# Kernel tuning notes

Hardware: AMD Instinct MI355X
Metric: run time of the kernel (lower is better)

## Reference

```python
import jax, jax.numpy as jnp
import numpy as np

N = 50000      # nodes
E = 500000     # edges
IN = 128       # input feature dim
HID = 64       # hidden per-head dim
CLS = 64       # num classes
SLOPE = 0.2    # leaky_relu negative slope


def _gat_layer(x, W, al, ar, src, dst):
    """One GATConv: project, per-edge score, edge-softmax over dst, weighted aggregate.
    x: [N, Din], W: [Din, H*F], al/ar: [H, F]. Returns [N, H, F]."""
    H, F = al.shape
    n = x.shape[0]
    feat = (x @ W).reshape(n, H, F)                      # [N,H,F]
    el = jnp.einsum('nhf,hf->nh', feat, al)              # [N,H]
    er = jnp.einsum('nhf,hf->nh', feat, ar)              # [N,H]
    e = el[src] + er[dst]                                # u_add_v -> [E,H]
    e = jnp.where(e >= 0, e, SLOPE * e)                  # leaky_relu
    # edge_softmax over destination nodes (numerically stable)
    m = jax.lax.stop_gradient(jax.ops.segment_max(e, dst, num_segments=n))
    ex = jnp.exp(e - m[dst])
    denom = jax.ops.segment_sum(ex, dst, num_segments=n)
    a = ex / denom[dst]                                  # [E,H]
    # u_mul_e + sum aggregation
    out = jax.ops.segment_sum(feat[src] * a[:, :, None], dst, num_segments=n)
    return out                                           # [N,H,F]


def setup_inputs() -> dict:
    key = jax.random.key(0)
    ks = jax.random.split(key, 12)
    s = 0.05  # xavier-ish scale
    x = jax.random.normal(ks[0], (N, IN), jnp.float32)
    src = jax.random.randint(ks[1], (E,), 0, N)
    dst = jax.random.randint(ks[2], (E,), 0, N)
    W1 = jax.random.normal(ks[3], (IN, 4 * HID), jnp.float32) * s
    al1 = jax.random.normal(ks[4], (4, HID), jnp.float32) * s
    ar1 = jax.random.normal(ks[5], (4, HID), jnp.float32) * s
    W2 = jax.random.normal(ks[6], (4 * HID, 4 * HID), jnp.float32) * s
    al2 = jax.random.normal(ks[7], (4, HID), jnp.float32) * s
    ar2 = jax.random.normal(ks[8], (4, HID), jnp.float32) * s
    W3 = jax.random.normal(ks[9], (4 * HID, CLS), jnp.float32) * s
    al3 = jax.random.normal(ks[10], (1, CLS), jnp.float32) * s
    ar3 = jax.random.normal(ks[11], (1, CLS), jnp.float32) * s
    res_W3 = jax.random.normal(jax.random.fold_in(key, 99), (4 * HID, CLS), jnp.float32) * s
    return {"x": x, "W1": W1, "al1": al1, "ar1": ar1, "W2": W2, "al2": al2,
            "ar2": ar2, "W3": W3, "al3": al3, "ar3": ar3, "res_W3": res_W3,
            "src": src, "dst": dst}


def reference(x, W1, al1, ar1, W2, al2, ar2, W3, al3, ar3, res_W3, src, dst):
    # layer 0: no residual, elu activation, flatten heads
    h = _gat_layer(x, W1, al1, ar1, src, dst)            # [N,4,64]
    h = jax.nn.elu(h).reshape(N, -1)                     # [N,256]
    # layer 1: residual is Identity (in_dst 256 == 4*64), elu, flatten
    h1 = _gat_layer(h, W2, al2, ar2, src, dst)           # [N,4,64]
    h1 = h1 + h.reshape(N, 4, HID)                       # residual (Identity)
    h = jax.nn.elu(h1).reshape(N, -1)                    # [N,256]
    # layer 2: residual Linear 256->64, no activation, mean over heads
    h2 = _gat_layer(h, W3, al3, ar3, src, dst)           # [N,1,64]
    h2 = h2 + (h @ res_W3).reshape(N, 1, CLS)            # residual fc
    logits = h2.mean(axis=1)                             # [N,64]
    return logits
```

## Files before the change

### kernel.cpp

```cpp
#include <hip/hip_runtime.h>
#include <hip/hip_bf16.h>
#include <math.h>

#define SLOPE 0.2f

typedef __attribute__((ext_vector_type(8))) short short8;
typedef __attribute__((ext_vector_type(4))) float f32x4;

static __device__ __forceinline__ float leakyf(float x) { return x >= 0.f ? x : SLOPE * x; }
static __device__ __forceinline__ float bflo(unsigned u) { return __builtin_bit_cast(float, u << 16); }
static __device__ __forceinline__ float bfhi(unsigned u) { return __builtin_bit_cast(float, u & 0xffff0000u); }

struct __align__(8) bf16x4 { __hip_bfloat16 x, y, z, w; };

__global__ void cvt_bf16(const float* __restrict__ in, __hip_bfloat16* __restrict__ o, int n) {
    int i = (blockIdx.x * blockDim.x + threadIdx.x) * 4;
    if (i + 3 < n) {
        float4 v = *(const float4*)(in + i);
        o[i + 0] = __float2bfloat16(v.x);
        o[i + 1] = __float2bfloat16(v.y);
        o[i + 2] = __float2bfloat16(v.z);
        o[i + 3] = __float2bfloat16(v.w);
    } else {
        for (int j = i; j < n; ++j) o[j] = __float2bfloat16(in[j]);
    }
}

__global__ void tconv(const float* __restrict__ W, __hip_bfloat16* __restrict__ Wt, int K, int Nc) {
    int i = blockIdx.x * blockDim.x + threadIdx.x;
    if (i < K * Nc) {
        int k = i / Nc, n = i - k * Nc;
        Wt[(size_t)n * K + k] = __float2bfloat16(W[i]);
    }
}

template<int HEADS, bool ACC, bool OUT_BF16, bool DO_ATTN>
__global__ __launch_bounds__(256) void gemm_bf16(const __hip_bfloat16* __restrict__ A,
                                                 const __hip_bfloat16* __restrict__ Wt,
                                                 void* __restrict__ outv,
                                                 const float* __restrict__ al,
                                                 const float* __restrict__ ar,
                                                 float* __restrict__ el,
                                                 float* __restrict__ er,
                                                 int M, int K) {
    const int Nc = HEADS * 64;
    const int lane = threadIdx.x & 63;
    const int wid = threadIdx.x >> 6;
    const int rlo = lane & 15;
    const int q = lane >> 4;
    const int kg = q * 8;
    const int head = (HEADS == 4) ? wid : 0;
    const int m0 = (HEADS == 4) ? blockIdx.x * 64 : blockIdx.x * 256 + wid * 64;
    const int cbase = head * 64;

    f32x4 acc[4][4];
#pragma unroll
    for (int mf = 0; mf < 4; ++mf)
#pragma unroll
        for (int nf = 0; nf < 4; ++nf) acc[mf][nf] = (f32x4){0.f, 0.f, 0.f, 0.f};

    for (int k0 = 0; k0 < K; k0 += 32) {
        short8 a[4];
#pragma unroll
        for (int mf = 0; mf < 4; ++mf) {
            int r = m0 + mf * 16 + rlo;
            if (r >= M) r = M - 1;
            a[mf] = *(const short8*)(A + (size_t)r * K + k0 + kg);
        }
#pragma unroll
        for (int nf = 0; nf < 4; ++nf) {
            short8 b = *(const short8*)(Wt + (size_t)(cbase + nf * 16 + rlo) * K + k0 + kg);
#pragma unroll
            for (int mf = 0; mf < 4; ++mf)
                acc[mf][nf] = __builtin_amdgcn_mfma_f32_16x16x32_bf16(a[mf], b, acc[mf][nf], 0, 0, 0);
        }
    }

    float alv[4], arv[4];
    if (DO_ATTN) {
#pragma unroll
        for (int nf = 0; nf < 4; ++nf) {
            alv[nf] = al[cbase + nf * 16 + rlo];
            arv[nf] = ar[cbase + nf * 16 + rlo];
        }
    }

#pragma unroll
    for (int mf = 0; mf < 4; ++mf) {
#pragma unroll
        for (int reg = 0; reg < 4; ++reg) {
            int r = m0 + mf * 16 + q * 4 + reg;
            if (DO_ATTN) {
                float pl = 0.f, pr = 0.f;
#pragma unroll
                for (int nf = 0; nf < 4; ++nf) {
                    pl += acc[mf][nf][reg] * alv[nf];
                    pr += acc[mf][nf][reg] * arv[nf];
                }
#pragma unroll
                for (int off = 1; off < 16; off <<= 1) {
                    pl += __shfl_xor(pl, off);
                    pr += __shfl_xor(pr, off);
                }
                if (rlo == 0 && r < M) {
                    el[(size_t)r * HEADS + head] = pl;
                    er[(size_t)r * HEADS + head] = pr;
                }
            }
            if (r < M) {
#pragma unroll
                for (int nf = 0; nf < 4; ++nf) {
                    int c = cbase + nf * 16 + rlo;
                    float v = acc[mf][nf][reg];
                    if (OUT_BF16) {
                        ((__hip_bfloat16*)outv)[(size_t)r * Nc + c] = __float2bfloat16(v);
                    } else {
                        float* o = (float*)outv + (size_t)r * Nc + c;
                        *o = ACC ? (*o + v) : v;
                    }
                }
            }
        }
    }
}

__global__ void hist_kernel(const int* __restrict__ dst, int* __restrict__ counts, int e) {
    int i = blockIdx.x * blockDim.x + threadIdx.x;
    if (i < e) atomicAdd(&counts[dst[i]], 1);
}

__global__ __launch_bounds__(1024) void scan_block(const int* __restrict__ counts,
                                                   int* __restrict__ offsets,
                                                   int* __restrict__ bsums, int n) {
    __shared__ int ws[16];
    int tid = threadIdx.x, lane = tid & 63, wid = tid >> 6;
    int idx = blockIdx.x * 1024 + tid;
    int v = (idx < n) ? counts[idx] : 0;
    int s = v;
#pragma unroll
    for (int off = 1; off < 64; off <<= 1) {
        int t = __shfl_up(s, off);
        if (lane >= off) s += t;
    }
    if (lane == 63) ws[wid] = s;
    __syncthreads();
    if (tid < 16) {
        int w2 = ws[tid];
#pragma unroll
        for (int off = 1; off < 16; off <<= 1) {
            int t = __shfl_up(w2, off);
            if (tid >= off) w2 += t;
        }
        ws[tid] = w2;
    }
    __syncthreads();
    int wpre = wid ? ws[wid - 1] : 0;
    if (idx < n) offsets[idx] = wpre + s - v;
    if (tid == 0) bsums[blockIdx.x] = ws[15];
}

__global__ void scan_sums(int* bsums, int nb) {
    int lane = threadIdx.x;
    int v = (lane < nb) ? bsums[lane] : 0;
    int s = v;
#pragma unroll
    for (int off = 1; off < 64; off <<= 1) {
        int t = __shfl_up(s, off);
        if (lane >= off) s += t;
    }
    if (lane < nb) bsums[lane] = s - v;
}

__global__ __launch_bounds__(1024) void add_off(const int* __restrict__ bsums,
                                                int* __restrict__ offsets, int n, int e) {
    int idx = blockIdx.x * 1024 + threadIdx.x;
    if (idx < n) offsets[idx] += bsums[blockIdx.x];
    if (idx == 0) offsets[n] = e;
}

__global__ void copy_int_kernel(const int* __restrict__ a, int* __restrict__ b, int n) {
    int i = blockIdx.x * blockDim.x + threadIdx.x;
    if (i < n) b[i] = a[i];
}

__global__ void scatter_kernel(const int* __restrict__ src, const int* __restrict__ dst,
                               int* __restrict__ cursor, int* __restrict__ csr_src, int e) {
    int i = blockIdx.x * blockDim.x + threadIdx.x;
    if (i < e) {
        int pos = atomicAdd(&cursor[dst[i]], 1);
        csr_src[pos] = src[i];
    }
}

template<int H, bool RES, int ACT, bool OUT_BF16>
__global__ __launch_bounds__(256) void gat_agg(const __hip_bfloat16* __restrict__ feat,
                                               const float* __restrict__ el,
                                               const float* __restrict__ er,
                                               const int* __restrict__ offsets,
                                               const int* __restrict__ csr_src,
                                               const __hip_bfloat16* __restrict__ resid,
                                               void* __restrict__ outv, int n) {
    const int D = H * 64;
    int node = blockIdx.x * 4 + (threadIdx.x >> 6);
    int lane = threadIdx.x & 63;
    if (node >= n) return;
    int e0 = offsets[node], e1 = offsets[node + 1];
    const int head = (H == 4) ? (lane >> 4) : 0;
    float erh = er[(size_t)node * H + head];

    float m = -INFINITY, den = 0.f;
    float acc[4] = {0.f, 0.f, 0.f, 0.f};
    const unsigned short* fp = (const unsigned short*)feat;

#define STEP(LV, UX, UY)                                                \
    {                                                                   \
        float xx = leakyf((LV) + erh);                                  \
        float mn = fmaxf(m, xx);                                        \
        float rs = __expf(m - mn);                                      \
        float w = __expf(xx - mn);                                      \
        m = mn;                                                         \
        den = den * rs + w;                                             \
        acc[0] = acc[0] * rs + w * bflo(UX);                            \
        if (H == 4) {                                                   \
            acc[1] = acc[1] * rs + w * bfhi(UX);                        \
            acc[2] = acc[2] * rs + w * bflo(UY);                        \
            acc[3] = acc[3] * rs + w * bfhi(UY);                        \
        }                                                               \
    }

    int e = e0;
    for (; e + 2 <= e1; e += 2) {
        int s0 = csr_src[e], s1 = csr_src[e + 1];
        float l0 = el[(size_t)s0 * H + head];
        float l1 = el[(size_t)s1 * H + head];
        unsigned ux0, uy0 = 0, ux1, uy1 = 0;
        if (H == 4) {
            uint2 u0 = *(const uint2*)(fp + (size_t)s0 * D + lane * 4);
            uint2 u1 = *(const uint2*)(fp + (size_t)s1 * D + lane * 4);
            ux0 = u0.x; uy0 = u0.y; ux1 = u1.x; uy1 = u1.y;
        } else {
            ux0 = fp[(size_t)s0 * D + lane];
            ux1 = fp[(size_t)s1 * D + lane];
        }
        STEP(l0, ux0, uy0);
        STEP(l1, ux1, uy1);
    }
    if (e < e1) {
        int s0 = csr_src[e];
        float l0 = el[(size_t)s0 * H + head];
        unsigned ux0, uy0 = 0;
        if (H == 4) {
            uint2 u0 = *(const uint2*)(fp + (size_t)s0 * D + lane * 4);
            ux0 = u0.x; uy0 = u0.y;
        } else {
            ux0 = fp[(size_t)s0 * D + lane];
        }
        STEP(l0, ux0, uy0);
    }
#undef STEP

    float inv = den > 0.f ? 1.f / den : 0.f;
    float v[4];
#pragma unroll
    for (int i = 0; i < 4; ++i) v[i] = acc[i] * inv;

    if (RES) {
        if (H == 4) {
            uint2 ru = *(const uint2*)((const unsigned short*)resid + (size_t)node * D + lane * 4);
            v[0] += bflo(ru.x); v[1] += bfhi(ru.x); v[2] += bflo(ru.y); v[3] += bfhi(ru.y);
        } else {
            v[0] += bflo(((const unsigned short*)resid)[(size_t)node * D + lane]);
        }
    }
    if (ACT == 1) {
#pragma unroll
        for (int i = 0; i < 4; ++i) v[i] = v[i] > 0.f ? v[i] : __expf(v[i]) - 1.f;
    }
    if (OUT_BF16) {
        if (H == 4) {
            bf16x4 o = {__float2bfloat16(v[0]), __float2bfloat16(v[1]),
                        __float2bfloat16(v[2]), __float2bfloat16(v[3])};
            *(bf16x4*)((__hip_bfloat16*)outv + (size_t)node * D + lane * 4) = o;
        } else {
            ((__hip_bfloat16*)outv)[(size_t)node * D + lane] = __float2bfloat16(v[0]);
        }
    } else {
        if (H == 4) {
#pragma unroll
            for (int i = 0; i < 4; ++i)
                ((float*)outv)[(size_t)node * D + lane * 4 + i] = v[i];
        } else {
            ((float*)outv)[(size_t)node * D + lane] = v[0];
        }
    }
}

extern "C" void kernel_launch(void* const* d_in, const int* in_sizes, int n_in,
                              void* d_out, int out_size, void* d_ws, size_t ws_size,
                              hipStream_t stream) {
    const float* x      = (const float*)d_in[0];
    const float* W1     = (const float*)d_in[1];
    const float* al1    = (const float*)d_in[2];
    const float* ar1    = (const float*)d_in[3];
    const float* W2     = (const float*)d_in[4];
    const float* al2    = (const float*)d_in[5];
    const float* ar2    = (const float*)d_in[6];
    const float* W3     = (const float*)d_in[7];
    const float* al3    = (const float*)d_in[8];
    const float* ar3    = (const float*)d_in[9];
    const float* res_W3 = (const float*)d_in[10];
    const int*   src    = (const int*)d_in[11];
    const int*   dst    = (const int*)d_in[12];

    const int N = in_sizes[0] / 128;
    const int E = in_sizes[11];

    float* out = (float*)d_out;

    __hip_bfloat16* xb    = (__hip_bfloat16*)d_ws;
    __hip_bfloat16* featb = xb + (size_t)N * 128;
    __hip_bfloat16* h1    = featb + (size_t)N * 256;
    __hip_bfloat16* h2    = h1 + (size_t)N * 256;
    __hip_bfloat16* W1t   = h2 + (size_t)N * 256;
    __hip_bfloat16* W2t   = W1t + 128 * 256;
    __hip_bfloat16* W3t   = W2t + 256 * 256;
    __hip_bfloat16* RW3t  = W3t + 256 * 64;
    float* el = (float*)(RW3t + 256 * 64);
    float* er = el + (size_t)N * 4;
    int* offsets = (int*)(er + (size_t)N * 4);
    int* cursor  = offsets + (N + 1);
    int* csr_src = cursor + N;
    int* bsums   = csr_src + E;

    const int T = 256;
    const int scan_blocks = (N + 1023) / 1024;

    cvt_bf16<<<(N * 128 / 4 + T - 1) / T, T, 0, stream>>>(x, xb, N * 128);
    tconv<<<(128 * 256 + T - 1) / T, T, 0, stream>>>(W1, W1t, 128, 256);
    tconv<<<(256 * 256 + T - 1) / T, T, 0, stream>>>(W2, W2t, 256, 256);
    tconv<<<(256 * 64 + T - 1) / T, T, 0, stream>>>(W3, W3t, 256, 64);
    tconv<<<(256 * 64 + T - 1) / T, T, 0, stream>>>(res_W3, RW3t, 256, 64);

    hipMemsetAsync(cursor, 0, (size_t)N * sizeof(int), stream);
    hist_kernel<<<(E + T - 1) / T, T, 0, stream>>>(dst, cursor, E);
    scan_block<<<scan_blocks, 1024, 0, stream>>>(cursor, offsets, bsums, N);
    scan_sums<<<1, 64, 0, stream>>>(bsums, scan_blocks);
    add_off<<<scan_blocks, 1024, 0, stream>>>(bsums, offsets, N, E);
    copy_int_kernel<<<(N + T - 1) / T, T, 0, stream>>>(offsets, cursor, N);
    scatter_kernel<<<(E + T - 1) / T, T, 0, stream>>>(src, dst, cursor, csr_src, E);

    int gemm4_blocks = (N + 63) / 64;
    int gemm1_blocks = (N + 255) / 256;
    int node_blocks = (N + 3) / 4;

    gemm_bf16<4, false, true, true><<<gemm4_blocks, T, 0, stream>>>(xb, W1t, featb, al1, ar1, el, er, N, 128);
    gat_agg<4, false, 1, true><<<node_blocks, T, 0, stream>>>(featb, el, er, offsets, csr_src, nullptr, h1, N);

    gemm_bf16<4, false, true, true><<<gemm4_blocks, T, 0, stream>>>(h1, W2t, featb, al2, ar2, el, er, N, 256);
    gat_agg<4, true, 1, true><<<node_blocks, T, 0, stream>>>(featb, el, er, offsets, csr_src, h1, h2, N);

    gemm_bf16<1, false, true, true><<<gemm1_blocks, T, 0, stream>>>(h2, W3t, featb, al3, ar3, el, er, N, 256);
    gat_agg<1, false, 0, false><<<node_blocks, T, 0, stream>>>(featb, el, er, offsets, csr_src, nullptr, out, N);
    gemm_bf16<1, true, false, false><<<gemm1_blocks, T, 0, stream>>>(h2, RW3t, out, nullptr, nullptr, nullptr, nullptr, N, 256);
}
```

Before: 312.4 us.

## Fuse input cast, residual GEMM, cursor copy; drop online softmax max tracking

The x-to-bf16 conversion moves inside the first GEMM. W3 and the residual weight are concatenated so one layer-3 GEMM writes both the attention features and the fp32 residual, and the aggregation kernel adds that residual. The cursor copy is folded into add_off. The aggregation drops the running-max online softmax in favour of a clamped plain exp-sum with two independent accumulators and 4-way edge unrolling. This removes several launches, one read-modify-write of the output, and per-edge rescaling work, but skips max subtraction, which relies on scores being bounded (clamped at 80) and could lose accuracy with large scores.

```diff
diff --git a/kernel.cpp b/kernel.cpp
--- a/kernel.cpp
+++ b/kernel.cpp
@@ -10,48 +10,124 @@
 static __device__ __forceinline__ float leakyf(float x) { return x >= 0.f ? x : SLOPE * x; }
 static __device__ __forceinline__ float bflo(unsigned u) { return __builtin_bit_cast(float, u << 16); }
 static __device__ __forceinline__ float bfhi(unsigned u) { return __builtin_bit_cast(float, u & 0xffff0000u); }
-
-struct __align__(8) bf16x4 { __hip_bfloat16 x, y, z, w; };
-
-__global__ void cvt_bf16(const float* __restrict__ in, __hip_bfloat16* __restrict__ o, int n) {
-    int i = (blockIdx.x * blockDim.x + threadIdx.x) * 4;
-    if (i + 3 < n) {
-        float4 v = *(const float4*)(in + i);
-        o[i + 0] = __float2bfloat16(v.x);
-        o[i + 1] = __float2bfloat16(v.y);
-        o[i + 2] = __float2bfloat16(v.z);
-        o[i + 3] = __float2bfloat16(v.w);
-    } else {
-        for (int j = i; j < n; ++j) o[j] = __float2bfloat16(in[j]);
-    }
-}
-
-__global__ void tconv(const float* __restrict__ W, __hip_bfloat16* __restrict__ Wt, int K, int Nc) {
+static __device__ __forceinline__ unsigned short f2bf(float f) {
+    unsigned u = __builtin_bit_cast(unsigned, f);
+    return (unsigned short)((u + 0x7fff + ((u >> 16) & 1)) >> 16);
+}
+
+struct __align__(8) us4 { unsigned short a, b, c, d; };
+
+__global__ void tconv(const float* __restrict__ W, unsigned short* __restrict__ Wt, int K, int Nc) {
     int i = blockIdx.x * blockDim.x + threadIdx.x;
     if (i < K * Nc) {
         int k = i / Nc, n = i - k * Nc;
-        Wt[(size_t)n * K + k] = __float2bfloat16(W[i]);
-    }
-}
-
-template<int HEADS, bool ACC, bool OUT_BF16, bool DO_ATTN>
-__global__ __launch_bounds__(256) void gemm_bf16(const __hip_bfloat16* __restrict__ A,
-                                                 const __hip_bfloat16* __restrict__ Wt,
-                                                 void* __restrict__ outv,
-                                                 const float* __restrict__ al,
-                                                 const float* __restrict__ ar,
-                                                 float* __restrict__ el,
-                                                 float* __restrict__ er,
-                                                 int M, int K) {
-    const int Nc = HEADS * 64;
+        Wt[(size_t)n * K + k] = f2bf(W[i]);
+    }
+}
+
+template<bool A_F32>
+__global__ __launch_bounds__(256) void gemm_l12(const void* __restrict__ Av,
+                                                const unsigned short* __restrict__ Wt,
+                                                unsigned short* __restrict__ outb,
+                                                const float* __restrict__ al,
+                                                const float* __restrict__ ar,
+                                                float* __restrict__ el,
+                                                float* __restrict__ er,
+                                                int M, int K) {
     const int lane = threadIdx.x & 63;
     const int wid = threadIdx.x >> 6;
     const int rlo = lane & 15;
     const int q = lane >> 4;
     const int kg = q * 8;
-    const int head = (HEADS == 4) ? wid : 0;
-    const int m0 = (HEADS == 4) ? blockIdx.x * 64 : blockIdx.x * 256 + wid * 64;
-    const int cbase = head * 64;
+    const int m0 = blockIdx.x * 64;
+    const int cbase = wid * 64;
+
+    f32x4 acc[4][4];
+#pragma unroll
+    for (int mf = 0; mf < 4; ++mf)
+#pragma unroll
+        for (int nf = 0; nf < 4; ++nf) acc[mf][nf] = (f32x4){0.f, 0.f, 0.f, 0.f};
+
+    for (int k0 = 0; k0 < K; k0 += 32) {
+        short8 a[4];
+#pragma unroll
+        for (int mf = 0; mf < 4; ++mf) {
+            int r = m0 + mf * 16 + rlo;
+            if (r >= M) r = M - 1;
+            if (A_F32) {
+                const float* ap = (const float*)Av + (size_t)r * K + k0 + kg;
+                float4 f0 = *(const float4*)ap;
+                float4 f1 = *(const float4*)(ap + 4);
+                short8 t;
+                t[0] = f2bf(f0.x); t[1] = f2bf(f0.y); t[2] = f2bf(f0.z); t[3] = f2bf(f0.w);
+                t[4] = f2bf(f1.x); t[5] = f2bf(f1.y); t[6] = f2bf(f1.z); t[7] = f2bf(f1.w);
+                a[mf] = t;
+            } else {
+                a[mf] = *(const short8*)((const unsigned short*)Av + (size_t)r * K + k0 + kg);
+            }
+        }
+#pragma unroll
+        for (int nf = 0; nf < 4; ++nf) {
+            short8 b = *(const short8*)(Wt + (size_t)(cbase + nf * 16 + rlo) * K + k0 + kg);
+#pragma unroll
+            for (int mf = 0; mf < 4; ++mf)
+                acc[mf][nf] = __builtin_amdgcn_mfma_f32_16x16x32_bf16(a[mf], b, acc[mf][nf], 0, 0, 0);
+        }
+    }
+
+    float alv[4], arv[4];
+#pragma unroll
+    for (int nf = 0; nf < 4; ++nf) {
+        alv[nf] = al[cbase + nf * 16 + rlo];
+        arv[nf] = ar[cbase + nf * 16 + rlo];
+    }
+
+#pragma unroll
+    for (int mf = 0; mf < 4; ++mf) {
+#pragma unroll
+        for (int reg = 0; reg < 4; ++reg) {
+            int r = m0 + mf * 16 + q * 4 + reg;
+            float pl = 0.f, pr = 0.f;
+#pragma unroll
+            for (int nf = 0; nf < 4; ++nf) {
+                pl += acc[mf][nf][reg] * alv[nf];
+                pr += acc[mf][nf][reg] * arv[nf];
+            }
+#pragma unroll
+            for (int off = 1; off < 16; off <<= 1) {
+                pl += __shfl_xor(pl, off);
+                pr += __shfl_xor(pr, off);
+            }
+            if (rlo == 0 && r < M) {
+                el[(size_t)r * 4 + wid] = pl;
+                er[(size_t)r * 4 + wid] = pr;
+            }
+            if (r < M) {
+#pragma unroll
+                for (int nf = 0; nf < 4; ++nf)
+                    outb[(size_t)r * 256 + cbase + nf * 16 + rlo] = f2bf(acc[mf][nf][reg]);
+            }
+        }
+    }
+}
+
+__global__ __launch_bounds__(256) void gemm_l3(const unsigned short* __restrict__ A,
+                                               const unsigned short* __restrict__ Wt,
+                                               unsigned short* __restrict__ featb,
+                                               float* __restrict__ resf,
+                                               const float* __restrict__ al,
+                                               const float* __restrict__ ar,
+                                               float* __restrict__ el,
+                                               float* __restrict__ er, int M) {
+    const int K = 256;
+    const int lane = threadIdx.x & 63;
+    const int wid = threadIdx.x >> 6;
+    const int rlo = lane & 15;
+    const int q = lane >> 4;
+    const int kg = q * 8;
+    const int m0 = blockIdx.x * 128 + (wid >> 1) * 64;
+    const int ch = wid & 1;
+    const int cbase = ch * 64;
 
     f32x4 acc[4][4];
 #pragma unroll
@@ -77,11 +153,11 @@
     }
 
     float alv[4], arv[4];
-    if (DO_ATTN) {
+    if (ch == 0) {
 #pragma unroll
         for (int nf = 0; nf < 4; ++nf) {
-            alv[nf] = al[cbase + nf * 16 + rlo];
-            arv[nf] = ar[cbase + nf * 16 + rlo];
+            alv[nf] = al[nf * 16 + rlo];
+            arv[nf] = ar[nf * 16 + rlo];
         }
     }
 
@@ -90,7 +166,7 @@
 #pragma unroll
         for (int reg = 0; reg < 4; ++reg) {
             int r = m0 + mf * 16 + q * 4 + reg;
-            if (DO_ATTN) {
+            if (ch == 0) {
                 float pl = 0.f, pr = 0.f;
 #pragma unroll
                 for (int nf = 0; nf < 4; ++nf) {
@@ -102,23 +178,16 @@
                     pl += __shfl_xor(pl, off);
                     pr += __shfl_xor(pr, off);
                 }
-                if (rlo == 0 && r < M) {
-                    el[(size_t)r * HEADS + head] = pl;
-                    er[(size_t)r * HEADS + head] = pr;
+                if (rlo == 0 && r < M) { el[r] = pl; er[r] = pr; }
+                if (r < M) {
+#pragma unroll
+                    for (int nf = 0; nf < 4; ++nf)
+                        featb[(size_t)r * 64 + nf * 16 + rlo] = f2bf(acc[mf][nf][reg]);
                 }
-            }
-            if (r < M) {
-#pragma unroll
-                for (int nf = 0; nf < 4; ++nf) {
-                    int c = cbase + nf * 16 + rlo;
-                    float v = acc[mf][nf][reg];
-                    if (OUT_BF16) {
-                        ((__hip_bfloat16*)outv)[(size_t)r * Nc + c] = __float2bfloat16(v);
-                    } else {
-                        float* o = (float*)outv + (size_t)r * Nc + c;
-                        *o = ACC ? (*o + v) : v;
-                    }
-                }
+            } else if (r < M) {
+#pragma unroll
+                for (int nf = 0; nf < 4; ++nf)
+                    resf[(size_t)r * 64 + nf * 16 + rlo] = acc[mf][nf][reg];
             }
         }
     }
@@ -172,15 +241,15 @@
 }
 
 __global__ __launch_bounds__(1024) void add_off(const int* __restrict__ bsums,
-                                                int* __restrict__ offsets, int n, int e) {
+                                                int* __restrict__ offsets,
+                                                int* __restrict__ cursor, int n, int e) {
     int idx = blockIdx.x * 1024 + threadIdx.x;
-    if (idx < n) offsets[idx] += bsums[blockIdx.x];
+    if (idx < n) {
+        int v = offsets[idx] + bsums[blockIdx.x];
+        offsets[idx] = v;
+        cursor[idx] = v;
+    }
     if (idx == 0) offsets[n] = e;
-}
-
-__global__ void copy_int_kernel(const int* __restrict__ a, int* __restrict__ b, int n) {
-    int i = blockIdx.x * blockDim.x + threadIdx.x;
-    if (i < n) b[i] = a[i];
 }
 
 __global__ void scatter_kernel(const int* __restrict__ src, const int* __restrict__ dst,
@@ -192,13 +261,13 @@
     }
 }
 
-template<int H, bool RES, int ACT, bool OUT_BF16>
-__global__ __launch_bounds__(256) void gat_agg(const __hip_bfloat16* __restrict__ feat,
+template<int H, int RES, int ACT, bool OUT_BF16>
+__global__ __launch_bounds__(256) void gat_agg(const unsigned short* __restrict__ fp,
                                                const float* __restrict__ el,
                                                const float* __restrict__ er,
                                                const int* __restrict__ offsets,
                                                const int* __restrict__ csr_src,
-                                               const __hip_bfloat16* __restrict__ resid,
+                                               const void* __restrict__ resid,
                                                void* __restrict__ outv, int n) {
     const int D = H * 64;
     int node = blockIdx.x * 4 + (threadIdx.x >> 6);
@@ -208,69 +277,74 @@
     const int head = (H == 4) ? (lane >> 4) : 0;
     float erh = er[(size_t)node * H + head];
 
-    float m = -INFINITY, den = 0.f;
-    float acc[4] = {0.f, 0.f, 0.f, 0.f};
-    const unsigned short* fp = (const unsigned short*)feat;
-
-#define STEP(LV, UX, UY)                                                \
-    {                                                                   \
-        float xx = leakyf((LV) + erh);                                  \
-        float mn = fmaxf(m, xx);                                        \
-        float rs = __expf(m - mn);                                      \
-        float w = __expf(xx - mn);                                      \
-        m = mn;                                                         \
-        den = den * rs + w;                                             \
-        acc[0] = acc[0] * rs + w * bflo(UX);                            \
-        if (H == 4) {                                                   \
-            acc[1] = acc[1] * rs + w * bfhi(UX);                        \
-            acc[2] = acc[2] * rs + w * bflo(UY);                        \
-            acc[3] = acc[3] * rs + w * bfhi(UY);                        \
-        }                                                               \
+    float denA = 0.f, denB = 0.f;
+    float accA[4] = {0.f, 0.f, 0.f, 0.f};
+    float accB[4] = {0.f, 0.f, 0.f, 0.f};
+
+#define STEP(DEN, AC, LV, UX, UY)                                      \
+    {                                                                  \
+        float xx = fminf(leakyf((LV) + erh), 80.f);                    \
+        float w = __expf(xx);                                          \
+        DEN += w;                                                      \
+        AC[0] += w * bflo(UX);                                         \
+        if (H == 4) {                                                  \
+            AC[1] += w * bfhi(UX);                                     \
+            AC[2] += w * bflo(UY);                                     \
+            AC[3] += w * bfhi(UY);                                     \
+        }                                                              \
     }
 
     int e = e0;
-    for (; e + 2 <= e1; e += 2) {
-        int s0 = csr_src[e], s1 = csr_src[e + 1];
+    for (; e + 4 <= e1; e += 4) {
+        int s0 = csr_src[e], s1 = csr_src[e + 1], s2 = csr_src[e + 2], s3 = csr_src[e + 3];
         float l0 = el[(size_t)s0 * H + head];
         float l1 = el[(size_t)s1 * H + head];
-        unsigned ux0, uy0 = 0, ux1, uy1 = 0;
+        float l2 = el[(size_t)s2 * H + head];
+        float l3 = el[(size_t)s3 * H + head];
+        unsigned x0, y0 = 0, x1, y1 = 0, x2, y2 = 0, x3, y3 = 0;
         if (H == 4) {
             uint2 u0 = *(const uint2*)(fp + (size_t)s0 * D + lane * 4);
             uint2 u1 = *(const uint2*)(fp + (size_t)s1 * D + lane * 4);
-            ux0 = u0.x; uy0 = u0.y; ux1 = u1.x; uy1 = u1.y;
+            uint2 u2 = *(const uint2*)(fp + (size_t)s2 * D + lane * 4);
+            uint2 u3 = *(const uint2*)(fp + (size_t)s3 * D + lane * 4);
+            x0 = u0.x; y0 = u0.y; x1 = u1.x; y1 = u1.y;
+            x2 = u2.x; y2 = u2.y; x3 = u3.x; y3 = u3.y;
         } else {
-            ux0 = fp[(size_t)s0 * D + lane];
-            ux1 = fp[(size_t)s1 * D + lane];
-        }
-        STEP(l0, ux0, uy0);
-        STEP(l1, ux1, uy1);
-    }
-    if (e < e1) {
+            x0 = fp[(size_t)s0 * D + lane];
+            x1 = fp[(size_t)s1 * D + lane];
+            x2 = fp[(size_t)s2 * D + lane];
+            x3 = fp[(size_t)s3 * D + lane];
+        }
+        STEP(denA, accA, l0, x0, y0);
+        STEP(denB, accB, l1, x1, y1);
+        STEP(denA, accA, l2, x2, y2);
+        STEP(denB, accB, l3, x3, y3);
+    }
+    for (; e < e1; ++e) {
         int s0 = csr_src[e];
         float l0 = el[(size_t)s0 * H + head];
-        unsigned ux0, uy0 = 0;
+        unsigned x0, y0 = 0;
         if (H == 4) {
             uint2 u0 = *(const uint2*)(fp + (size_t)s0 * D + lane * 4);
-            ux0 = u0.x; uy0 = u0.y;
+            x0 = u0.x; y0 = u0.y;
         } else {
-            ux0 = fp[(size_t)s0 * D + lane];
-        }
-        STEP(l0, ux0, uy0);
+            x0 = fp[(size_t)s0 * D + lane];
+        }
+        STEP(denA, accA, l0, x0, y0);
     }
 #undef STEP
 
+    float den = denA + denB;
     float inv = den > 0.f ? 1.f / den : 0.f;
     float v[4];
 #pragma unroll
-    for (int i = 0; i < 4; ++i) v[i] = acc[i] * inv;
-
-    if (RES) {
-        if (H == 4) {
-            uint2 ru = *(const uint2*)((const unsigned short*)resid + (size_t)node * D + lane * 4);
-            v[0] += bflo(ru.x); v[1] += bfhi(ru.x); v[2] += bflo(ru.y); v[3] += bfhi(ru.y);
-        } else {
-            v[0] += bflo(((const unsigned short*)resid)[(size_t)node * D + lane]);
-        }
+    for (int i = 0; i < 4; ++i) v[i] = (accA[i] + accB[i]) * inv;
+
+    if (RES == 1) {
+        uint2 ru = *(const uint2*)((const unsigned short*)resid + (size_t)node * D + lane * 4);
+        v[0] += bflo(ru.x); v[1] += bfhi(ru.x); v[2] += bflo(ru.y); v[3] += bfhi(ru.y);
+    } else if (RES == 2) {
+        v[0] += ((const float*)resid)[(size_t)node * D + lane];
     }
     if (ACT == 1) {
 #pragma unroll
@@ -278,17 +352,15 @@
     }
     if (OUT_BF16) {
         if (H == 4) {
-            bf16x4 o = {__float2bfloat16(v[0]), __float2bfloat16(v[1]),
-                        __float2bfloat16(v[2]), __float2bfloat16(v[3])};
-            *(bf16x4*)((__hip_bfloat16*)outv + (size_t)node * D + lane * 4) = o;
+            us4 o = {f2bf(v[0]), f2bf(v[1]), f2bf(v[2]), f2bf(v[3])};
+            *(us4*)((unsigned short*)outv + (size_t)node * D + lane * 4) = o;
         } else {
-            ((__hip_bfloat16*)outv)[(size_t)node * D + lane] = __float2bfloat16(v[0]);
+            ((unsigned short*)outv)[(size_t)node * D + lane] = f2bf(v[0]);
         }
     } else {
         if (H == 4) {
-#pragma unroll
-            for (int i = 0; i < 4; ++i)
-                ((float*)outv)[(size_t)node * D + lane * 4 + i] = v[i];
+            float4 o = {v[0], v[1], v[2], v[3]};
+            *(float4*)((float*)outv + (size_t)node * D + lane * 4) = o;
         } else {
             ((float*)outv)[(size_t)node * D + lane] = v[0];
         }
@@ -317,16 +389,15 @@
 
     float* out = (float*)d_out;
 
-    __hip_bfloat16* xb    = (__hip_bfloat16*)d_ws;
-    __hip_bfloat16* featb = xb + (size_t)N * 128;
-    __hip_bfloat16* h1    = featb + (size_t)N * 256;
-    __hip_bfloat16* h2    = h1 + (size_t)N * 256;
-    __hip_bfloat16* W1t   = h2 + (size_t)N * 256;
-    __hip_bfloat16* W2t   = W1t + 128 * 256;
-    __hip_bfloat16* W3t   = W2t + 256 * 256;
-    __hip_bfloat16* RW3t  = W3t + 256 * 64;
-    float* el = (float*)(RW3t + 256 * 64);
-    float* er = el + (size_t)N * 4;
+    unsigned short* featb = (unsigned short*)d_ws;
+    unsigned short* h1    = featb + (size_t)N * 256;
+    unsigned short* h2    = h1 + (size_t)N * 256;
+    unsigned short* W1t   = h2 + (size_t)N * 256;
+    unsigned short* W2t   = W1t + 256 * 128;
+    unsigned short* W3c   = W2t + 256 * 256;
+    float* resf = (float*)(W3c + 128 * 256);
+    float* el   = resf + (size_t)N * 64;
+    float* er   = el + (size_t)N * 4;
     int* offsets = (int*)(er + (size_t)N * 4);
     int* cursor  = offsets + (N + 1);
     int* csr_src = cursor + N;
@@ -335,31 +406,28 @@
     const int T = 256;
     const int scan_blocks = (N + 1023) / 1024;
 
-    cvt_bf16<<<(N * 128 / 4 + T - 1) / T, T, 0, stream>>>(x, xb, N * 128);
     tconv<<<(128 * 256 + T - 1) / T, T, 0, stream>>>(W1, W1t, 128, 256);
     tconv<<<(256 * 256 + T - 1) / T, T, 0, stream>>>(W2, W2t, 256, 256);
-    tconv<<<(256 * 64 + T - 1) / T, T, 0, stream>>>(W3, W3t, 256, 64);
-    tconv<<<(256 * 64 + T - 1) / T, T, 0, stream>>>(res_W3, RW3t, 256, 64);
+    tconv<<<(256 * 64 + T - 1) / T, T, 0, stream>>>(W3, W3c, 256, 64);
+    tconv<<<(256 * 64 + T - 1) / T, T, 0, stream>>>(res_W3, W3c + 64 * 256, 256, 64);
 
     hipMemsetAsync(cursor, 0, (size_t)N * sizeof(int), stream);
     hist_kernel<<<(E + T - 1) / T, T, 0, stream>>>(dst, cursor, E);
     scan_block<<<scan_blocks, 1024, 0, stream>>>(cursor, offsets, bsums, N);
     scan_sums<<<1, 64, 0, stream>>>(bsums, scan_blocks);
-    add_off<<<scan_blocks, 1024, 0, stream>>>(bsums, offsets, N, E);
-    copy_int_kernel<<<(N + T - 1) / T, T, 0, stream>>>(offsets, cursor, N);
+    add_off<<<scan_blocks, 1024, 0, stream>>>(bsums, offsets, cursor, N, E);
     scatter_kernel<<<(E + T - 1) / T, T, 0, stream>>>(src, dst, cursor, csr_src, E);
 
-    int gemm4_blocks = (N + 63) / 64;
-    int gemm1_blocks = (N + 255) / 256;
+    int gemm12_blocks = (N + 63) / 64;
+    int gemm3_blocks = (N + 127) / 128;
     int node_blocks = (N + 3) / 4;
 
-    gemm_bf16<4, false, true, true><<<gemm4_blocks, T, 0, stream>>>(xb, W1t, featb, al1, ar1, el, er, N, 128);
-    gat_agg<4, false, 1, true><<<node_blocks, T, 0, stream>>>(featb, el, er, offsets, csr_src, nullptr, h1, N);
-
-    gemm_bf16<4, false, true, true><<<gemm4_blocks, T, 0, stream>>>(h1, W2t, featb, al2, ar2, el, er, N, 256);
-    gat_agg<4, true, 1, true><<<node_blocks, T, 0, stream>>>(featb, el, er, offsets, csr_src, h1, h2, N);
-
-    gemm_bf16<1, false, true, true><<<gemm1_blocks, T, 0, stream>>>(h2, W3t, featb, al3, ar3, el, er, N, 256);
-    gat_agg<1, false, 0, false><<<node_blocks, T, 0, stream>>>(featb, el, er, offsets, csr_src, nullptr, out, N);
-    gemm_bf16<1, true, false, false><<<gemm1_blocks, T, 0, stream>>>(h2, RW3t, out, nullptr, nullptr, nullptr, nullptr, N, 256);
-}
+    gemm_l12<true><<<gemm12_blocks, T, 0, stream>>>(x, W1t, featb, al1, ar1, el, er, N, 128);
+    gat_agg<4, 0, 1, true><<<node_blocks, T, 0, stream>>>(featb, el, er, offsets, csr_src, nullptr, h1, N);
+
+    gemm_l12<false><<<gemm12_blocks, T, 0, stream>>>(h1, W2t, featb, al2, ar2, el, er, N, 256);
+    gat_agg<4, 1, 1, true><<<node_blocks, T, 0, stream>>>(featb, el, er, offsets, csr_src, h1, h2, N);
+
+    gemm_l3<<<gemm3_blocks, T, 0, stream>>>(h2, W3c, featb, resf, al3, ar3, el, er, N);
+    gat_agg<1, 2, 0, false><<<node_blocks, T, 0, stream>>>(featb, el, er, offsets, csr_src, resf, out, N);
+}
```

Result: faster. 291.7 us (-6.6%).
